# Performance work log

Measured on AMD Instinct MI355X. Metric: run time of the kernel, lower is better.

The kernel has to match this reference:

```python
import jax, jax.numpy as jnp
import numpy as np

B, H, S, D = 1, 8, 4096, 64


def setup_inputs() -> dict:
    key = jax.random.key(0)
    kq, kk, kv = jax.random.split(key, 3)
    Q = jax.random.normal(kq, (B, H, S, D), dtype=jnp.float32)
    K = jax.random.normal(kk, (B, H, S, D), dtype=jnp.float32)
    V = jax.random.normal(kv, (B, H, S, D), dtype=jnp.float32)
    # causal mask: 1 where attention allowed, 0 where blocked (matches masked_fill(mask==0, -inf))
    mask = jnp.tril(jnp.ones((S, S), dtype=jnp.int32))[None, None, :, :]
    return {"Q": Q, "K": K, "V": V, "mask": mask}


def reference(Q, K, V, mask):
    d_k = Q.shape[-1]
    scale = 1.0 / jnp.sqrt(jnp.asarray(d_k, Q.dtype))
    # [B,H,S,S] attention scores
    attn_score = jnp.einsum("bhqd,bhkd->bhqk", Q, K) * scale
    neg_inf = jnp.asarray(-jnp.inf, attn_score.dtype)
    attn_score = jnp.where(mask == 0, neg_inf, attn_score)
    attn_weight = jax.nn.softmax(attn_score, axis=-1)
    attn_output = jnp.einsum("bhqk,bhkd->bhqd", attn_weight, V)
    return attn_output
```

## Files before the change

### kernel.cpp

```cpp
#include <hip/hip_runtime.h>

#define S_LEN 4096
#define NHEAD 8
#define DDIM  64
#define NT    64
#define TILE_BYTES 8192
#define WS_NEEDED (2ull * NHEAD * NT * TILE_BYTES)

typedef __attribute__((ext_vector_type(4))) float f32x4;
typedef __attribute__((ext_vector_type(2))) float f32x2;
typedef __attribute__((ext_vector_type(8))) short bf16x8;

__device__ __forceinline__ unsigned cvt_pk(float lo, float hi) {
  unsigned r;
  asm("v_cvt_pk_bf16_f32 %0, %1, %2" : "=v"(r) : "v"(lo), "v"(hi));
  return r;
}
__device__ __forceinline__ float ex2(float x) {
  float r;
  asm("v_exp_f32 %0, %1" : "=v"(r) : "v"(x));
  return r;
}
__device__ __forceinline__ unsigned short f2bf(float f) {
  unsigned u = __float_as_uint(f);
  return (unsigned short)((u + 0x7fffu + ((u >> 16) & 1u)) >> 16);
}
__device__ __forceinline__ unsigned pk2(float a, float b) {
  return (unsigned)f2bf(a) | ((unsigned)f2bf(b) << 16);
}

__global__ __launch_bounds__(256)
void prepass(const float* __restrict__ K, const float* __restrict__ V,
             char* __restrict__ wsK, char* __restrict__ wsV) {
  const int bid = blockIdx.x;
  const int h = bid & 7, t = bid >> 3;
  const int tid = threadIdx.x;
  const size_t base = ((size_t)h * S_LEN + t * 64) * DDIM;
  char* ck = wsK + (size_t)(h * NT + t) * TILE_BYTES;
  char* cv = wsV + (size_t)(h * NT + t) * TILE_BYTES;
  {
    const int key = tid >> 2;
    const int fn = key >> 4, lq = key & 15;
#pragma unroll
    for (int p = 0; p < 2; ++p) {
      const int du = (tid & 3) + p * 4;
      const int kk = du >> 2, g = du & 3;
      const float* src = K + base + (size_t)key * DDIM + du * 8;
      f32x4 a = *(const f32x4*)src;
      f32x4 b = *(const f32x4*)(src + 4);
      uint4 u = {cvt_pk(a[0], a[1]), cvt_pk(a[2], a[3]),
                 cvt_pk(b[0], b[1]), cvt_pk(b[2], b[3])};
      *(uint4*)(ck + kk * 4096 + fn * 1024 + g * 256 + lq * 16) = u;
    }
  }
  {
    const int kgrp = tid >> 5;
    const int d0 = (tid & 31) * 2;
    const int kk = kgrp >> 2, g = kgrp & 3;
    float va[8], vb[8];
#pragma unroll
    for (int jj = 0; jj < 8; ++jj) {
      f32x2 x = *(const f32x2*)(V + base + (size_t)(kgrp * 8 + jj) * DDIM + d0);
      va[jj] = x[0]; vb[jj] = x[1];
    }
    uint4 ua = {cvt_pk(va[0], va[1]), cvt_pk(va[2], va[3]),
                cvt_pk(va[4], va[5]), cvt_pk(va[6], va[7])};
    uint4 ub = {cvt_pk(vb[0], vb[1]), cvt_pk(vb[2], vb[3]),
                cvt_pk(vb[4], vb[5]), cvt_pk(vb[6], vb[7])};
    const int fm0 = d0 >> 4, lq0 = d0 & 15;
    const int fm1 = (d0 + 1) >> 4, lq1 = (d0 + 1) & 15;
    *(uint4*)(cv + kk * 4096 + fm0 * 1024 + g * 256 + lq0 * 16) = ua;
    *(uint4*)(cv + kk * 4096 + fm1 * 1024 + g * 256 + lq1 * 16) = ub;
  }
}

__global__ __launch_bounds__(256)
void attn_fwd10(const float* __restrict__ Q, const char* __restrict__ wsK,
                const char* __restrict__ wsV, float* __restrict__ O) {
  __shared__ __align__(16) char pool[25344];

  const int tid = threadIdx.x, wave = tid >> 6, lane = tid & 63;
  const int g = lane >> 4, lq = lane & 15;
  const int bid = blockIdx.x, h = bid & 7, i = bid >> 3;
  const int qc = 127 - i;
  const int jd = qc >> 1;
  const int qbase = qc * 32;
  const int n = (jd >= wave) ? ((jd - wave) >> 2) + 1 : 0;

  const char* tK = wsK + (size_t)h * NT * TILE_BYTES;
  const char* tV = wsV + (size_t)h * NT * TILE_BYTES;
  const int foff = lane * 16;

  const float qsc = 0.125f * 1.44269504088896340736f;
  bf16x8 qf[2][2];
#pragma unroll
  for (int qh = 0; qh < 2; ++qh) {
    const float* qp = Q + ((size_t)h * S_LEN + qbase + qh * 16 + lq) * DDIM + g * 8;
#pragma unroll
    for (int kk = 0; kk < 2; ++kk) {
      f32x4 a = *(const f32x4*)(qp + kk * 32);
      f32x4 b = *(const f32x4*)(qp + kk * 32 + 4);
      uint4 u = {cvt_pk(a[0] * qsc, a[1] * qsc), cvt_pk(a[2] * qsc, a[3] * qsc),
                 cvt_pk(b[0] * qsc, b[1] * qsc), cvt_pk(b[2] * qsc, b[3] * qsc)};
      qf[qh][kk] = __builtin_bit_cast(bf16x8, u);
    }
  }

  f32x4 of0[4], of1[4];
#pragma unroll
  for (int fm = 0; fm < 4; ++fm) { of0[fm] = (f32x4){0,0,0,0}; of1[fm] = (f32x4){0,0,0,0}; }
  float l0 = 0.f, l1 = 0.f;

  char* pbase = pool + wave * 4608;
  const int prow = lq * 72;

  bf16x8 kf[4][2];
  if (n > 0) {
    const char* pk = tK + (size_t)wave * TILE_BYTES + foff;
#pragma unroll
    for (int fn = 0; fn < 4; ++fn)
#pragma unroll
      for (int kk = 0; kk < 2; ++kk)
        kf[fn][kk] = *(const bf16x8*)(pk + kk * 4096 + fn * 1024);
  }

  int j = wave;
  for (int it = 0; it < n; ++it, j += 4) {
    bf16x8 vf[4][2];
    const char* pv = tV + (size_t)j * TILE_BYTES + foff;
#pragma unroll
    for (int fm = 0; fm < 4; ++fm)
#pragma unroll
      for (int kk = 0; kk < 2; ++kk)
        vf[fm][kk] = *(const bf16x8*)(pv + kk * 4096 + fm * 1024);

    f32x4 s0[4], s1[4];
#pragma unroll
    for (int fn = 0; fn < 4; ++fn) {
      f32x4 a = (f32x4){0,0,0,0}, b = (f32x4){0,0,0,0};
      a = __builtin_amdgcn_mfma_f32_16x16x32_bf16(kf[fn][0], qf[0][0], a, 0, 0, 0);
      a = __builtin_amdgcn_mfma_f32_16x16x32_bf16(kf[fn][1], qf[0][1], a, 0, 0, 0);
      b = __builtin_amdgcn_mfma_f32_16x16x32_bf16(kf[fn][0], qf[1][0], b, 0, 0, 0);
      b = __builtin_amdgcn_mfma_f32_16x16x32_bf16(kf[fn][1], qf[1][1], b, 0, 0, 0);
      s0[fn] = a; s1[fn] = b;
    }

    if (it + 1 < n) {
      const char* pk = tK + (size_t)(j + 4) * TILE_BYTES + foff;
#pragma unroll
      for (int fn = 0; fn < 4; ++fn)
#pragma unroll
        for (int kk = 0; kk < 2; ++kk)
          kf[fn][kk] = *(const bf16x8*)(pk + kk * 4096 + fn * 1024);
    }

    if (j == jd) {
      const int koff = qbase - jd * 64;
#pragma unroll
      for (int fn = 0; fn < 4; ++fn)
#pragma unroll
        for (int rr = 0; rr < 4; ++rr) {
          const int key = fn * 16 + g * 4 + rr;
          if (key > koff + lq)      s0[fn][rr] = -__builtin_inff();
          if (key > koff + 16 + lq) s1[fn][rr] = -__builtin_inff();
        }
    }

    float rs0 = 0.f, rs1 = 0.f;
#pragma unroll
    for (int fn = 0; fn < 4; ++fn) {
      float a00 = ex2(s0[fn][0]), a01 = ex2(s0[fn][1]);
      float a02 = ex2(s0[fn][2]), a03 = ex2(s0[fn][3]);
      float a10 = ex2(s1[fn][0]), a11 = ex2(s1[fn][1]);
      float a12 = ex2(s1[fn][2]), a13 = ex2(s1[fn][3]);
      s0[fn][0] = a00; s0[fn][1] = a01; s0[fn][2] = a02; s0[fn][3] = a03;
      s1[fn][0] = a10; s1[fn][1] = a11; s1[fn][2] = a12; s1[fn][3] = a13;
      rs0 += (a00 + a01) + (a02 + a03);
      rs1 += (a10 + a11) + (a12 + a13);
    }
    l0 += rs0; l1 += rs1;

#pragma unroll
    for (int fn = 0; fn < 4; ++fn) {
      const int kk = fn >> 1;
      const int boff = ((fn & 1) * 2 + (g >> 1)) * 16 + (g & 1) * 8;
      unsigned long long w0 = (unsigned long long)cvt_pk(s0[fn][0], s0[fn][1])
                            | ((unsigned long long)cvt_pk(s0[fn][2], s0[fn][3]) << 32);
      unsigned long long w1 = (unsigned long long)cvt_pk(s1[fn][0], s1[fn][1])
                            | ((unsigned long long)cvt_pk(s1[fn][2], s1[fn][3]) << 32);
      *(unsigned long long*)(pbase + (kk * 2 + 0) * 1152 + prow + boff) = w0;
      *(unsigned long long*)(pbase + (kk * 2 + 1) * 1152 + prow + boff) = w1;
    }
    asm volatile("s_waitcnt lgkmcnt(0)" ::: "memory");

#pragma unroll
    for (int kk = 0; kk < 2; ++kk) {
      bf16x8 p0 = *(const bf16x8*)(pbase + (kk * 2 + 0) * 1152 + prow + g * 16);
      bf16x8 p1 = *(const bf16x8*)(pbase + (kk * 2 + 1) * 1152 + prow + g * 16);
#pragma unroll
      for (int fm = 0; fm < 4; ++fm) {
        of0[fm] = __builtin_amdgcn_mfma_f32_16x16x32_bf16(vf[fm][kk], p0, of0[fm], 0, 0, 0);
        of1[fm] = __builtin_amdgcn_mfma_f32_16x16x32_bf16(vf[fm][kk], p1, of1[fm], 0, 0, 0);
      }
    }
  }

  l0 += __shfl_xor(l0, 16); l0 += __shfl_xor(l0, 32);
  l1 += __shfl_xor(l1, 16); l1 += __shfl_xor(l1, 32);

  __syncthreads();
  if (wave < 3) {
    char* mb = pool + wave * 8192;
#pragma unroll
    for (int fm = 0; fm < 4; ++fm) {
      *(f32x4*)(mb + (fm * 2 + 0) * 1024 + g * 256 + lq * 16) = of0[fm];
      *(f32x4*)(mb + (fm * 2 + 1) * 1024 + g * 256 + lq * 16) = of1[fm];
    }
    if (g == 0) {
      f32x4 v = {l0, l1, 0.f, 0.f};
      *(f32x4*)(pool + 24576 + wave * 256 + lq * 16) = v;
    }
  }
  __syncthreads();
  if (wave == 3) {
    float den0 = l0, den1 = l1;
#pragma unroll
    for (int a = 0; a < 3; ++a) {
      f32x4 ml = *(const f32x4*)(pool + 24576 + a * 256 + lq * 16);
      den0 += ml[0];
      den1 += ml[1];
    }
    const float inv0 = 1.f / den0, inv1 = 1.f / den1;
    float* o0 = O + ((size_t)h * S_LEN + qbase + lq) * DDIM + g * 4;
    float* o1 = o0 + 16 * DDIM;
#pragma unroll
    for (int fm = 0; fm < 4; ++fm) {
      f32x4 r0 = of0[fm], r1 = of1[fm];
#pragma unroll
      for (int a = 0; a < 3; ++a) {
        r0 += *(const f32x4*)(pool + a * 8192 + (fm * 2 + 0) * 1024 + g * 256 + lq * 16);
        r1 += *(const f32x4*)(pool + a * 8192 + (fm * 2 + 1) * 1024 + g * 256 + lq * 16);
      }
      *(f32x4*)(o0 + fm * 16) = r0 * inv0;
      *(f32x4*)(o1 + fm * 16) = r1 * inv1;
    }
  }
}

__global__ __launch_bounds__(256, 2)
void attn_fwd_v1(const float* __restrict__ Q, const float* __restrict__ K,
                 const float* __restrict__ V, float* __restrict__ O) {
  __shared__ __align__(16) char kl[64 * 128];
  __shared__ __align__(16) char vt[64 * 128];
  __shared__ __align__(16) char pl[4 * 16 * 128];
  const int tid = threadIdx.x, wave = tid >> 6, lane = tid & 63;
  const int g = lane >> 4, lq = lane & 15;
  const int bid = blockIdx.x, h = bid & 7, i = bid >> 3;
  const int qt = (i & 1) ? (63 - (i >> 1)) : (i >> 1);
  const int qw = qt * 64 + wave * 16 + lq;
  const float* Qh = Q + ((size_t)h * S_LEN + qw) * DDIM;
  const float* Kh = K + (size_t)h * S_LEN * DDIM;
  const float* Vh = V + (size_t)h * S_LEN * DDIM;
  bf16x8 qf[2];
#pragma unroll
  for (int kk = 0; kk < 2; ++kk) {
    const float* p = Qh + g * 8 + kk * 32;
    f32x4 a = *(const f32x4*)p;
    f32x4 b = *(const f32x4*)(p + 4);
#pragma unroll
    for (int jj = 0; jj < 4; ++jj) {
      qf[kk][jj]     = (short)f2bf(a[jj] * 0.125f);
      qf[kk][jj + 4] = (short)f2bf(b[jj] * 0.125f);
    }
  }
  f32x4 of[4];
#pragma unroll
  for (int fm = 0; fm < 4; ++fm) of[fm] = (f32x4){0.f, 0.f, 0.f, 0.f};
  float mrun = -__builtin_inff(), lrun = 0.f;
  const int r16 = tid >> 4, c4 = tid & 15;
  const int vc = tid & 63, vkb = (tid >> 6) * 4;
  for (int j = 0; j <= qt; ++j) {
    const int k0 = j * 64;
    __syncthreads();
#pragma unroll
    for (int p = 0; p < 4; ++p) {
      const int rr = p * 16 + r16;
      f32x4 x = *(const f32x4*)(Kh + (size_t)(k0 + rr) * DDIM + c4 * 4);
      unsigned long long w = (unsigned long long)pk2(x[0], x[1])
                           | ((unsigned long long)pk2(x[2], x[3]) << 32);
      *(unsigned long long*)(kl + rr * 128 + ((c4 * 8) ^ ((rr & 7) << 4))) = w;
    }
#pragma unroll
    for (int p = 0; p < 4; ++p) {
      const int key = vkb + p * 16;
      const float* vp = Vh + (size_t)(k0 + key) * DDIM + vc;
      float v0 = vp[0], v1 = vp[DDIM], v2 = vp[2 * DDIM], v3 = vp[3 * DDIM];
      unsigned long long w = (unsigned long long)pk2(v0, v1)
                           | ((unsigned long long)pk2(v2, v3) << 32);
      *(unsigned long long*)(vt + vc * 128 + ((key * 2) ^ ((vc & 7) << 4))) = w;
    }
    __syncthreads();
    f32x4 sf[4];
#pragma unroll
    for (int fn = 0; fn < 4; ++fn) {
      f32x4 sv = (f32x4){0.f, 0.f, 0.f, 0.f};
#pragma unroll
      for (int kk = 0; kk < 2; ++kk) {
        const int krow = fn * 16 + lq;
        bf16x8 a = *(const bf16x8*)(kl + krow * 128 +
                                    ((g * 16 + kk * 64) ^ ((krow & 7) << 4)));
        sv = __builtin_amdgcn_mfma_f32_16x16x32_bf16(a, qf[kk], sv, 0, 0, 0);
      }
      sf[fn] = sv;
    }
    if (j == qt) {
      const int qrel = wave * 16 + lq;
#pragma unroll
      for (int fn = 0; fn < 4; ++fn)
#pragma unroll
        for (int rr = 0; rr < 4; ++rr)
          if (fn * 16 + g * 4 + rr > qrel) sf[fn][rr] = -__builtin_inff();
    }
    float mt = -__builtin_inff();
#pragma unroll
    for (int fn = 0; fn < 4; ++fn)
#pragma unroll
      for (int rr = 0; rr < 4; ++rr) mt = fmaxf(mt, sf[fn][rr]);
    mt = fmaxf(mt, __shfl_xor(mt, 16));
    mt = fmaxf(mt, __shfl_xor(mt, 32));
    const float mnew = fmaxf(mrun, mt);
    const float alpha = __expf(mrun - mnew);
    float rs = 0.f;
#pragma unroll
    for (int fn = 0; fn < 4; ++fn)
#pragma unroll
      for (int rr = 0; rr < 4; ++rr) {
        float p = __expf(sf[fn][rr] - mnew);
        sf[fn][rr] = p;
        rs += p;
      }
    rs += __shfl_xor(rs, 16);
    rs += __shfl_xor(rs, 32);
    mrun = mnew;
    lrun = lrun * alpha + rs;
#pragma unroll
    for (int fm = 0; fm < 4; ++fm) of[fm] *= alpha;
#pragma unroll
    for (int fn = 0; fn < 4; ++fn) {
      unsigned long long w = (unsigned long long)pk2(sf[fn][0], sf[fn][1])
                           | ((unsigned long long)pk2(sf[fn][2], sf[fn][3]) << 32);
      *(unsigned long long*)(pl + wave * 2048 + lq * 128 +
                             ((fn * 32 + g * 8) ^ ((lq & 7) << 4))) = w;
    }
    asm volatile("s_waitcnt lgkmcnt(0)" ::: "memory");
#pragma unroll
    for (int fm = 0; fm < 4; ++fm) {
#pragma unroll
      for (int kk = 0; kk < 2; ++kk) {
        const int vrow = fm * 16 + lq;
        bf16x8 av = *(const bf16x8*)(vt + vrow * 128 +
                                     ((g * 16 + kk * 64) ^ ((vrow & 7) << 4)));
        bf16x8 bp = *(const bf16x8*)(pl + wave * 2048 + lq * 128 +
                                     ((g * 16 + kk * 64) ^ ((lq & 7) << 4)));
        of[fm] = __builtin_amdgcn_mfma_f32_16x16x32_bf16(av, bp, of[fm], 0, 0, 0);
      }
    }
  }
  const float inv = 1.0f / lrun;
  float* orow = O + ((size_t)h * S_LEN + qw) * DDIM;
#pragma unroll
  for (int fm = 0; fm < 4; ++fm) {
    f32x4 o = of[fm] * inv;
    *(f32x4*)(orow + fm * 16 + g * 4) = o;
  }
}

extern "C" void kernel_launch(void* const* d_in, const int* in_sizes, int n_in,
                              void* d_out, int out_size, void* d_ws, size_t ws_size,
                              hipStream_t stream) {
  (void)in_sizes; (void)n_in; (void)out_size;
  const float* Q = (const float*)d_in[0];
  const float* K = (const float*)d_in[1];
  const float* V = (const float*)d_in[2];
  float* O = (float*)d_out;
  if (ws_size >= WS_NEEDED) {
    char* wsK = (char*)d_ws;
    char* wsV = wsK + (size_t)NHEAD * NT * TILE_BYTES;
    prepass<<<dim3(512), dim3(256), 0, stream>>>(K, V, wsK, wsV);
    attn_fwd10<<<dim3(1024), dim3(256), 0, stream>>>(Q, wsK, wsV, O);
  } else {
    attn_fwd_v1<<<dim3(512), dim3(256), 0, stream>>>(Q, K, V, O);
  }
}
```

Before: 44.30 us.

## Split causal attention KV range across two blocks and merge partials

Each 32-query chunk's key range is split into two halves processed by separate blocks (2048 blocks total). Each block writes unnormalized partial outputs and row sums to a workspace slot, and a new merge kernel sums the two partials and normalizes. The goal is to shorten the longest blocks on the causal tail and improve load balance and CU occupancy. The cost is an extra kernel launch plus a partial-result write and read through global memory. Because the kernel uses a fixed, shared exponent with no running max, partials can be summed directly without rescaling.

```diff
diff --git a/kernel.cpp b/kernel.cpp
--- a/kernel.cpp
+++ b/kernel.cpp
@@ -5,7 +5,10 @@
 #define DDIM  64
 #define NT    64
 #define TILE_BYTES 8192
-#define WS_NEEDED (2ull * NHEAD * NT * TILE_BYTES)
+#define SLOT_BYTES 8448
+#define NSEG 2048
+#define WS_KV (2ull * NHEAD * NT * TILE_BYTES)
+#define WS_SPLIT (WS_KV + (unsigned long long)NSEG * SLOT_BYTES)
 
 typedef __attribute__((ext_vector_type(4))) float f32x4;
 typedef __attribute__((ext_vector_type(2))) float f32x2;
@@ -20,13 +23,6 @@
   float r;
   asm("v_exp_f32 %0, %1" : "=v"(r) : "v"(x));
   return r;
-}
-__device__ __forceinline__ unsigned short f2bf(float f) {
-  unsigned u = __float_as_uint(f);
-  return (unsigned short)((u + 0x7fffu + ((u >> 16) & 1u)) >> 16);
-}
-__device__ __forceinline__ unsigned pk2(float a, float b) {
-  return (unsigned)f2bf(a) | ((unsigned)f2bf(b) << 16);
 }
 
 __global__ __launch_bounds__(256)
@@ -75,17 +71,23 @@
 }
 
 __global__ __launch_bounds__(256)
-void attn_fwd10(const float* __restrict__ Q, const char* __restrict__ wsK,
-                const char* __restrict__ wsV, float* __restrict__ O) {
+void attn_fwd11(const float* __restrict__ Q, const char* __restrict__ wsK,
+                const char* __restrict__ wsV, char* __restrict__ wsP) {
   __shared__ __align__(16) char pool[25344];
 
   const int tid = threadIdx.x, wave = tid >> 6, lane = tid & 63;
   const int g = lane >> 4, lq = lane & 15;
-  const int bid = blockIdx.x, h = bid & 7, i = bid >> 3;
-  const int qc = 127 - i;
+  const int bid = blockIdx.x;
+  const int h = bid & 7, idx = bid >> 3;
+  const int qc = 127 - (idx >> 1), half = idx & 1;
   const int jd = qc >> 1;
+  const int T = jd + 1;
+  const int Th = (T + 1) >> 1;
+  const int h0 = half ? Th : 0;
+  const int hend = half ? T : Th;
   const int qbase = qc * 32;
-  const int n = (jd >= wave) ? ((jd - wave) >> 2) + 1 : 0;
+  const int rem = hend - h0 - wave;
+  const int n = (rem > 0) ? ((rem + 3) >> 2) : 0;
 
   const char* tK = wsK + (size_t)h * NT * TILE_BYTES;
   const char* tV = wsV + (size_t)h * NT * TILE_BYTES;
@@ -116,7 +118,7 @@
 
   bf16x8 kf[4][2];
   if (n > 0) {
-    const char* pk = tK + (size_t)wave * TILE_BYTES + foff;
+    const char* pk = tK + (size_t)(h0 + wave) * TILE_BYTES + foff;
 #pragma unroll
     for (int fn = 0; fn < 4; ++fn)
 #pragma unroll
@@ -124,7 +126,7 @@
         kf[fn][kk] = *(const bf16x8*)(pk + kk * 4096 + fn * 1024);
   }
 
-  int j = wave;
+  int j = h0 + wave;
   for (int it = 0; it < n; ++it, j += 4) {
     bf16x8 vf[4][2];
     const char* pv = tV + (size_t)j * TILE_BYTES + foff;
@@ -230,6 +232,189 @@
       den0 += ml[0];
       den1 += ml[1];
     }
+    char* slot = wsP + (size_t)bid * SLOT_BYTES;
+#pragma unroll
+    for (int fm = 0; fm < 4; ++fm) {
+      f32x4 r0 = of0[fm], r1 = of1[fm];
+#pragma unroll
+      for (int a = 0; a < 3; ++a) {
+        r0 += *(const f32x4*)(pool + a * 8192 + (fm * 2 + 0) * 1024 + g * 256 + lq * 16);
+        r1 += *(const f32x4*)(pool + a * 8192 + (fm * 2 + 1) * 1024 + g * 256 + lq * 16);
+      }
+      const int d = (fm * 16 + g * 4) * 4;
+      *(f32x4*)(slot + lq * 256 + d) = r0;
+      *(f32x4*)(slot + (16 + lq) * 256 + d) = r1;
+    }
+    if (g == 0) {
+      *(float*)(slot + 8192 + lq * 4) = den0;
+      *(float*)(slot + 8192 + (16 + lq) * 4) = den1;
+    }
+  }
+}
+
+__global__ __launch_bounds__(256)
+void mergek(const char* __restrict__ wsP, float* __restrict__ O) {
+  const int mb = blockIdx.x;
+  const int h = mb & 7, c = mb >> 3;
+  const int qc = 127 - c;
+  const char* s0 = wsP + (size_t)(c * 16 + h) * SLOT_BYTES;
+  const char* s1 = s0 + 8 * SLOT_BYTES;
+  const int t = threadIdx.x;
+  const int q = t >> 3, d0 = (t & 7) * 8;
+  const float l = *(const float*)(s0 + 8192 + q * 4)
+                + *(const float*)(s1 + 8192 + q * 4);
+  const float inv = 1.f / l;
+  const int off = q * 256 + d0 * 4;
+  f32x4 a0 = *(const f32x4*)(s0 + off);
+  f32x4 a1 = *(const f32x4*)(s1 + off);
+  f32x4 b0 = *(const f32x4*)(s0 + off + 16);
+  f32x4 b1 = *(const f32x4*)(s1 + off + 16);
+  float* o = O + ((size_t)h * S_LEN + qc * 32 + q) * DDIM + d0;
+  *(f32x4*)o = (a0 + a1) * inv;
+  *(f32x4*)(o + 4) = (b0 + b1) * inv;
+}
+
+__global__ __launch_bounds__(256)
+void attn_fwd10(const float* __restrict__ Q, const char* __restrict__ wsK,
+                const char* __restrict__ wsV, float* __restrict__ O) {
+  __shared__ __align__(16) char pool[25344];
+  const int tid = threadIdx.x, wave = tid >> 6, lane = tid & 63;
+  const int g = lane >> 4, lq = lane & 15;
+  const int bid = blockIdx.x, h = bid & 7, i = bid >> 3;
+  const int qc = 127 - i;
+  const int jd = qc >> 1;
+  const int qbase = qc * 32;
+  const int n = (jd >= wave) ? ((jd - wave) >> 2) + 1 : 0;
+  const char* tK = wsK + (size_t)h * NT * TILE_BYTES;
+  const char* tV = wsV + (size_t)h * NT * TILE_BYTES;
+  const int foff = lane * 16;
+  const float qsc = 0.125f * 1.44269504088896340736f;
+  bf16x8 qf[2][2];
+#pragma unroll
+  for (int qh = 0; qh < 2; ++qh) {
+    const float* qp = Q + ((size_t)h * S_LEN + qbase + qh * 16 + lq) * DDIM + g * 8;
+#pragma unroll
+    for (int kk = 0; kk < 2; ++kk) {
+      f32x4 a = *(const f32x4*)(qp + kk * 32);
+      f32x4 b = *(const f32x4*)(qp + kk * 32 + 4);
+      uint4 u = {cvt_pk(a[0] * qsc, a[1] * qsc), cvt_pk(a[2] * qsc, a[3] * qsc),
+                 cvt_pk(b[0] * qsc, b[1] * qsc), cvt_pk(b[2] * qsc, b[3] * qsc)};
+      qf[qh][kk] = __builtin_bit_cast(bf16x8, u);
+    }
+  }
+  f32x4 of0[4], of1[4];
+#pragma unroll
+  for (int fm = 0; fm < 4; ++fm) { of0[fm] = (f32x4){0,0,0,0}; of1[fm] = (f32x4){0,0,0,0}; }
+  float l0 = 0.f, l1 = 0.f;
+  char* pbase = pool + wave * 4608;
+  const int prow = lq * 72;
+  bf16x8 kf[4][2];
+  if (n > 0) {
+    const char* pk = tK + (size_t)wave * TILE_BYTES + foff;
+#pragma unroll
+    for (int fn = 0; fn < 4; ++fn)
+#pragma unroll
+      for (int kk = 0; kk < 2; ++kk)
+        kf[fn][kk] = *(const bf16x8*)(pk + kk * 4096 + fn * 1024);
+  }
+  int j = wave;
+  for (int it = 0; it < n; ++it, j += 4) {
+    bf16x8 vf[4][2];
+    const char* pv = tV + (size_t)j * TILE_BYTES + foff;
+#pragma unroll
+    for (int fm = 0; fm < 4; ++fm)
+#pragma unroll
+      for (int kk = 0; kk < 2; ++kk)
+        vf[fm][kk] = *(const bf16x8*)(pv + kk * 4096 + fm * 1024);
+    f32x4 s0[4], s1[4];
+#pragma unroll
+    for (int fn = 0; fn < 4; ++fn) {
+      f32x4 a = (f32x4){0,0,0,0}, b = (f32x4){0,0,0,0};
+      a = __builtin_amdgcn_mfma_f32_16x16x32_bf16(kf[fn][0], qf[0][0], a, 0, 0, 0);
+      a = __builtin_amdgcn_mfma_f32_16x16x32_bf16(kf[fn][1], qf[0][1], a, 0, 0, 0);
+      b = __builtin_amdgcn_mfma_f32_16x16x32_bf16(kf[fn][0], qf[1][0], b, 0, 0, 0);
+      b = __builtin_amdgcn_mfma_f32_16x16x32_bf16(kf[fn][1], qf[1][1], b, 0, 0, 0);
+      s0[fn] = a; s1[fn] = b;
+    }
+    if (it + 1 < n) {
+      const char* pk = tK + (size_t)(j + 4) * TILE_BYTES + foff;
+#pragma unroll
+      for (int fn = 0; fn < 4; ++fn)
+#pragma unroll
+        for (int kk = 0; kk < 2; ++kk)
+          kf[fn][kk] = *(const bf16x8*)(pk + kk * 4096 + fn * 1024);
+    }
+    if (j == jd) {
+      const int koff = qbase - jd * 64;
+#pragma unroll
+      for (int fn = 0; fn < 4; ++fn)
+#pragma unroll
+        for (int rr = 0; rr < 4; ++rr) {
+          const int key = fn * 16 + g * 4 + rr;
+          if (key > koff + lq)      s0[fn][rr] = -__builtin_inff();
+          if (key > koff + 16 + lq) s1[fn][rr] = -__builtin_inff();
+        }
+    }
+    float rs0 = 0.f, rs1 = 0.f;
+#pragma unroll
+    for (int fn = 0; fn < 4; ++fn) {
+      float a00 = ex2(s0[fn][0]), a01 = ex2(s0[fn][1]);
+      float a02 = ex2(s0[fn][2]), a03 = ex2(s0[fn][3]);
+      float a10 = ex2(s1[fn][0]), a11 = ex2(s1[fn][1]);
+      float a12 = ex2(s1[fn][2]), a13 = ex2(s1[fn][3]);
+      s0[fn][0] = a00; s0[fn][1] = a01; s0[fn][2] = a02; s0[fn][3] = a03;
+      s1[fn][0] = a10; s1[fn][1] = a11; s1[fn][2] = a12; s1[fn][3] = a13;
+      rs0 += (a00 + a01) + (a02 + a03);
+      rs1 += (a10 + a11) + (a12 + a13);
+    }
+    l0 += rs0; l1 += rs1;
+#pragma unroll
+    for (int fn = 0; fn < 4; ++fn) {
+      const int kk = fn >> 1;
+      const int boff = ((fn & 1) * 2 + (g >> 1)) * 16 + (g & 1) * 8;
+      unsigned long long w0 = (unsigned long long)cvt_pk(s0[fn][0], s0[fn][1])
+                            | ((unsigned long long)cvt_pk(s0[fn][2], s0[fn][3]) << 32);
+      unsigned long long w1 = (unsigned long long)cvt_pk(s1[fn][0], s1[fn][1])
+                            | ((unsigned long long)cvt_pk(s1[fn][2], s1[fn][3]) << 32);
+      *(unsigned long long*)(pbase + (kk * 2 + 0) * 1152 + prow + boff) = w0;
+      *(unsigned long long*)(pbase + (kk * 2 + 1) * 1152 + prow + boff) = w1;
+    }
+    asm volatile("s_waitcnt lgkmcnt(0)" ::: "memory");
+#pragma unroll
+    for (int kk = 0; kk < 2; ++kk) {
+      bf16x8 p0 = *(const bf16x8*)(pbase + (kk * 2 + 0) * 1152 + prow + g * 16);
+      bf16x8 p1 = *(const bf16x8*)(pbase + (kk * 2 + 1) * 1152 + prow + g * 16);
+#pragma unroll
+      for (int fm = 0; fm < 4; ++fm) {
+        of0[fm] = __builtin_amdgcn_mfma_f32_16x16x32_bf16(vf[fm][kk], p0, of0[fm], 0, 0, 0);
+        of1[fm] = __builtin_amdgcn_mfma_f32_16x16x32_bf16(vf[fm][kk], p1, of1[fm], 0, 0, 0);
+      }
+    }
+  }
+  l0 += __shfl_xor(l0, 16); l0 += __shfl_xor(l0, 32);
+  l1 += __shfl_xor(l1, 16); l1 += __shfl_xor(l1, 32);
+  __syncthreads();
+  if (wave < 3) {
+    char* mb = pool + wave * 8192;
+#pragma unroll
+    for (int fm = 0; fm < 4; ++fm) {
+      *(f32x4*)(mb + (fm * 2 + 0) * 1024 + g * 256 + lq * 16) = of0[fm];
+      *(f32x4*)(mb + (fm * 2 + 1) * 1024 + g * 256 + lq * 16) = of1[fm];
+    }
+    if (g == 0) {
+      f32x4 v = {l0, l1, 0.f, 0.f};
+      *(f32x4*)(pool + 24576 + wave * 256 + lq * 16) = v;
+    }
+  }
+  __syncthreads();
+  if (wave == 3) {
+    float den0 = l0, den1 = l1;
+#pragma unroll
+    for (int a = 0; a < 3; ++a) {
+      f32x4 ml = *(const f32x4*)(pool + 24576 + a * 256 + lq * 16);
+      den0 += ml[0];
+      den1 += ml[1];
+    }
     const float inv0 = 1.f / den0, inv1 = 1.f / den1;
     float* o0 = O + ((size_t)h * S_LEN + qbase + lq) * DDIM + g * 4;
     float* o1 = o0 + 16 * DDIM;
@@ -244,134 +429,6 @@
       *(f32x4*)(o0 + fm * 16) = r0 * inv0;
       *(f32x4*)(o1 + fm * 16) = r1 * inv1;
     }
-  }
-}
-
-__global__ __launch_bounds__(256, 2)
-void attn_fwd_v1(const float* __restrict__ Q, const float* __restrict__ K,
-                 const float* __restrict__ V, float* __restrict__ O) {
-  __shared__ __align__(16) char kl[64 * 128];
-  __shared__ __align__(16) char vt[64 * 128];
-  __shared__ __align__(16) char pl[4 * 16 * 128];
-  const int tid = threadIdx.x, wave = tid >> 6, lane = tid & 63;
-  const int g = lane >> 4, lq = lane & 15;
-  const int bid = blockIdx.x, h = bid & 7, i = bid >> 3;
-  const int qt = (i & 1) ? (63 - (i >> 1)) : (i >> 1);
-  const int qw = qt * 64 + wave * 16 + lq;
-  const float* Qh = Q + ((size_t)h * S_LEN + qw) * DDIM;
-  const float* Kh = K + (size_t)h * S_LEN * DDIM;
-  const float* Vh = V + (size_t)h * S_LEN * DDIM;
-  bf16x8 qf[2];
-#pragma unroll
-  for (int kk = 0; kk < 2; ++kk) {
-    const float* p = Qh + g * 8 + kk * 32;
-    f32x4 a = *(const f32x4*)p;
-    f32x4 b = *(const f32x4*)(p + 4);
-#pragma unroll
-    for (int jj = 0; jj < 4; ++jj) {
-      qf[kk][jj]     = (short)f2bf(a[jj] * 0.125f);
-      qf[kk][jj + 4] = (short)f2bf(b[jj] * 0.125f);
-    }
-  }
-  f32x4 of[4];
-#pragma unroll
-  for (int fm = 0; fm < 4; ++fm) of[fm] = (f32x4){0.f, 0.f, 0.f, 0.f};
-  float mrun = -__builtin_inff(), lrun = 0.f;
-  const int r16 = tid >> 4, c4 = tid & 15;
-  const int vc = tid & 63, vkb = (tid >> 6) * 4;
-  for (int j = 0; j <= qt; ++j) {
-    const int k0 = j * 64;
-    __syncthreads();
-#pragma unroll
-    for (int p = 0; p < 4; ++p) {
-      const int rr = p * 16 + r16;
-      f32x4 x = *(const f32x4*)(Kh + (size_t)(k0 + rr) * DDIM + c4 * 4);
-      unsigned long long w = (unsigned long long)pk2(x[0], x[1])
-                           | ((unsigned long long)pk2(x[2], x[3]) << 32);
-      *(unsigned long long*)(kl + rr * 128 + ((c4 * 8) ^ ((rr & 7) << 4))) = w;
-    }
-#pragma unroll
-    for (int p = 0; p < 4; ++p) {
-      const int key = vkb + p * 16;
-      const float* vp = Vh + (size_t)(k0 + key) * DDIM + vc;
-      float v0 = vp[0], v1 = vp[DDIM], v2 = vp[2 * DDIM], v3 = vp[3 * DDIM];
-      unsigned long long w = (unsigned long long)pk2(v0, v1)
-                           | ((unsigned long long)pk2(v2, v3) << 32);
-      *(unsigned long long*)(vt + vc * 128 + ((key * 2) ^ ((vc & 7) << 4))) = w;
-    }
-    __syncthreads();
-    f32x4 sf[4];
-#pragma unroll
-    for (int fn = 0; fn < 4; ++fn) {
-      f32x4 sv = (f32x4){0.f, 0.f, 0.f, 0.f};
-#pragma unroll
-      for (int kk = 0; kk < 2; ++kk) {
-        const int krow = fn * 16 + lq;
-        bf16x8 a = *(const bf16x8*)(kl + krow * 128 +
-                                    ((g * 16 + kk * 64) ^ ((krow & 7) << 4)));
-        sv = __builtin_amdgcn_mfma_f32_16x16x32_bf16(a, qf[kk], sv, 0, 0, 0);
-      }
-      sf[fn] = sv;
-    }
-    if (j == qt) {
-      const int qrel = wave * 16 + lq;
-#pragma unroll
-      for (int fn = 0; fn < 4; ++fn)
-#pragma unroll
-        for (int rr = 0; rr < 4; ++rr)
-          if (fn * 16 + g * 4 + rr > qrel) sf[fn][rr] = -__builtin_inff();
-    }
-    float mt = -__builtin_inff();
-#pragma unroll
-    for (int fn = 0; fn < 4; ++fn)
-#pragma unroll
-      for (int rr = 0; rr < 4; ++rr) mt = fmaxf(mt, sf[fn][rr]);
-    mt = fmaxf(mt, __shfl_xor(mt, 16));
-    mt = fmaxf(mt, __shfl_xor(mt, 32));
-    const float mnew = fmaxf(mrun, mt);
-    const float alpha = __expf(mrun - mnew);
-    float rs = 0.f;
-#pragma unroll
-    for (int fn = 0; fn < 4; ++fn)
-#pragma unroll
-      for (int rr = 0; rr < 4; ++rr) {
-        float p = __expf(sf[fn][rr] - mnew);
-        sf[fn][rr] = p;
-        rs += p;
-      }
-    rs += __shfl_xor(rs, 16);
-    rs += __shfl_xor(rs, 32);
-    mrun = mnew;
-    lrun = lrun * alpha + rs;
-#pragma unroll
-    for (int fm = 0; fm < 4; ++fm) of[fm] *= alpha;
-#pragma unroll
-    for (int fn = 0; fn < 4; ++fn) {
-      unsigned long long w = (unsigned long long)pk2(sf[fn][0], sf[fn][1])
-                           | ((unsigned long long)pk2(sf[fn][2], sf[fn][3]) << 32);
-      *(unsigned long long*)(pl + wave * 2048 + lq * 128 +
-                             ((fn * 32 + g * 8) ^ ((lq & 7) << 4))) = w;
-    }
-    asm volatile("s_waitcnt lgkmcnt(0)" ::: "memory");
-#pragma unroll
-    for (int fm = 0; fm < 4; ++fm) {
-#pragma unroll
-      for (int kk = 0; kk < 2; ++kk) {
-        const int vrow = fm * 16 + lq;
-        bf16x8 av = *(const bf16x8*)(vt + vrow * 128 +
-                                     ((g * 16 + kk * 64) ^ ((vrow & 7) << 4)));
-        bf16x8 bp = *(const bf16x8*)(pl + wave * 2048 + lq * 128 +
-                                     ((g * 16 + kk * 64) ^ ((lq & 7) << 4)));
-        of[fm] = __builtin_amdgcn_mfma_f32_16x16x32_bf16(av, bp, of[fm], 0, 0, 0);
-      }
-    }
-  }
-  const float inv = 1.0f / lrun;
-  float* orow = O + ((size_t)h * S_LEN + qw) * DDIM;
-#pragma unroll
-  for (int fm = 0; fm < 4; ++fm) {
-    f32x4 o = of[fm] * inv;
-    *(f32x4*)(orow + fm * 16 + g * 4) = o;
   }
 }
 
@@ -383,12 +440,15 @@
   const float* K = (const float*)d_in[1];
   const float* V = (const float*)d_in[2];
   float* O = (float*)d_out;
-  if (ws_size >= WS_NEEDED) {
-    char* wsK = (char*)d_ws;
-    char* wsV = wsK + (size_t)NHEAD * NT * TILE_BYTES;
+  char* wsK = (char*)d_ws;
+  char* wsV = wsK + (size_t)NHEAD * NT * TILE_BYTES;
+  char* wsP = wsK + WS_KV;
+  if (ws_size >= WS_SPLIT) {
+    prepass<<<dim3(512), dim3(256), 0, stream>>>(K, V, wsK, wsV);
+    attn_fwd11<<<dim3(NSEG), dim3(256), 0, stream>>>(Q, wsK, wsV, wsP);
+    mergek<<<dim3(1024), dim3(256), 0, stream>>>(wsP, O);
+  } else {
     prepass<<<dim3(512), dim3(256), 0, stream>>>(K, V, wsK, wsV);
     attn_fwd10<<<dim3(1024), dim3(256), 0, stream>>>(Q, wsK, wsV, O);
-  } else {
-    attn_fwd_v1<<<dim3(512), dim3(256), 0, stream>>>(Q, K, V, O);
-  }
-}
+  }
+}
```

After: 53.34 us. +20.4%, slower.

## Software-pipeline QK^T of next tile with softmax and PV of current tile

Applied to the files above, without the earlier changes.

Restructures the per-wave loop so the S=QK^T MFMAs for the next key tile are issued before the PV MFMAs of the current tile. The K prefetch moves two tiles ahead and the V load moves one iteration ahead. This overlaps MFMA work with the exp/convert/LDS staging and hides global load latency. In exchange, more registers stay live (s0/s1 and the vf/kf prefetch buffers), which may lower occupancy or cause spills.

```diff
diff --git a/kernel.cpp b/kernel.cpp
--- a/kernel.cpp
+++ b/kernel.cpp
@@ -75,7 +75,7 @@
 }
 
 __global__ __launch_bounds__(256)
-void attn_fwd10(const float* __restrict__ Q, const char* __restrict__ wsK,
+void attn_fwd13(const float* __restrict__ Q, const char* __restrict__ wsK,
                 const char* __restrict__ wsV, float* __restrict__ O) {
   __shared__ __align__(16) char pool[25344];
 
@@ -114,27 +114,19 @@
   char* pbase = pool + wave * 4608;
   const int prow = lq * 72;
 
-  bf16x8 kf[4][2];
+  bf16x8 kf[4][2], vf[4][2];
+  f32x4 s0[4], s1[4];
+
   if (n > 0) {
     const char* pk = tK + (size_t)wave * TILE_BYTES + foff;
+    const char* pv = tV + (size_t)wave * TILE_BYTES + foff;
 #pragma unroll
     for (int fn = 0; fn < 4; ++fn)
 #pragma unroll
-      for (int kk = 0; kk < 2; ++kk)
+      for (int kk = 0; kk < 2; ++kk) {
         kf[fn][kk] = *(const bf16x8*)(pk + kk * 4096 + fn * 1024);
-  }
-
-  int j = wave;
-  for (int it = 0; it < n; ++it, j += 4) {
-    bf16x8 vf[4][2];
-    const char* pv = tV + (size_t)j * TILE_BYTES + foff;
-#pragma unroll
-    for (int fm = 0; fm < 4; ++fm)
-#pragma unroll
-      for (int kk = 0; kk < 2; ++kk)
-        vf[fm][kk] = *(const bf16x8*)(pv + kk * 4096 + fm * 1024);
-
-    f32x4 s0[4], s1[4];
+        vf[fn][kk] = *(const bf16x8*)(pv + kk * 4096 + fn * 1024);
+      }
 #pragma unroll
     for (int fn = 0; fn < 4; ++fn) {
       f32x4 a = (f32x4){0,0,0,0}, b = (f32x4){0,0,0,0};
@@ -144,15 +136,18 @@
       b = __builtin_amdgcn_mfma_f32_16x16x32_bf16(kf[fn][1], qf[1][1], b, 0, 0, 0);
       s0[fn] = a; s1[fn] = b;
     }
-
-    if (it + 1 < n) {
-      const char* pk = tK + (size_t)(j + 4) * TILE_BYTES + foff;
+    if (n > 1) {
+      const char* pk2 = tK + (size_t)(wave + 4) * TILE_BYTES + foff;
 #pragma unroll
       for (int fn = 0; fn < 4; ++fn)
 #pragma unroll
         for (int kk = 0; kk < 2; ++kk)
-          kf[fn][kk] = *(const bf16x8*)(pk + kk * 4096 + fn * 1024);
-    }
+          kf[fn][kk] = *(const bf16x8*)(pk2 + kk * 4096 + fn * 1024);
+    }
+  }
+
+  int j = wave;
+  for (int it = 0; it < n; ++it, j += 4) {
 
     if (j == jd) {
       const int koff = qbase - jd * 64;
@@ -173,24 +168,31 @@
       float a02 = ex2(s0[fn][2]), a03 = ex2(s0[fn][3]);
       float a10 = ex2(s1[fn][0]), a11 = ex2(s1[fn][1]);
       float a12 = ex2(s1[fn][2]), a13 = ex2(s1[fn][3]);
-      s0[fn][0] = a00; s0[fn][1] = a01; s0[fn][2] = a02; s0[fn][3] = a03;
-      s1[fn][0] = a10; s1[fn][1] = a11; s1[fn][2] = a12; s1[fn][3] = a13;
       rs0 += (a00 + a01) + (a02 + a03);
       rs1 += (a10 + a11) + (a12 + a13);
-    }
-    l0 += rs0; l1 += rs1;
-
-#pragma unroll
-    for (int fn = 0; fn < 4; ++fn) {
       const int kk = fn >> 1;
       const int boff = ((fn & 1) * 2 + (g >> 1)) * 16 + (g & 1) * 8;
-      unsigned long long w0 = (unsigned long long)cvt_pk(s0[fn][0], s0[fn][1])
-                            | ((unsigned long long)cvt_pk(s0[fn][2], s0[fn][3]) << 32);
-      unsigned long long w1 = (unsigned long long)cvt_pk(s1[fn][0], s1[fn][1])
-                            | ((unsigned long long)cvt_pk(s1[fn][2], s1[fn][3]) << 32);
+      unsigned long long w0 = (unsigned long long)cvt_pk(a00, a01)
+                            | ((unsigned long long)cvt_pk(a02, a03) << 32);
+      unsigned long long w1 = (unsigned long long)cvt_pk(a10, a11)
+                            | ((unsigned long long)cvt_pk(a12, a13) << 32);
       *(unsigned long long*)(pbase + (kk * 2 + 0) * 1152 + prow + boff) = w0;
       *(unsigned long long*)(pbase + (kk * 2 + 1) * 1152 + prow + boff) = w1;
     }
+    l0 += rs0; l1 += rs1;
+
+    if (it + 1 < n) {
+#pragma unroll
+      for (int fn = 0; fn < 4; ++fn) {
+        f32x4 a = (f32x4){0,0,0,0}, b = (f32x4){0,0,0,0};
+        a = __builtin_amdgcn_mfma_f32_16x16x32_bf16(kf[fn][0], qf[0][0], a, 0, 0, 0);
+        a = __builtin_amdgcn_mfma_f32_16x16x32_bf16(kf[fn][1], qf[0][1], a, 0, 0, 0);
+        b = __builtin_amdgcn_mfma_f32_16x16x32_bf16(kf[fn][0], qf[1][0], b, 0, 0, 0);
+        b = __builtin_amdgcn_mfma_f32_16x16x32_bf16(kf[fn][1], qf[1][1], b, 0, 0, 0);
+        s0[fn] = a; s1[fn] = b;
+      }
+    }
+
     asm volatile("s_waitcnt lgkmcnt(0)" ::: "memory");
 
 #pragma unroll
@@ -201,6 +203,23 @@
       for (int fm = 0; fm < 4; ++fm) {
         of0[fm] = __builtin_amdgcn_mfma_f32_16x16x32_bf16(vf[fm][kk], p0, of0[fm], 0, 0, 0);
         of1[fm] = __builtin_amdgcn_mfma_f32_16x16x32_bf16(vf[fm][kk], p1, of1[fm], 0, 0, 0);
+      }
+    }
+
+    if (it + 1 < n) {
+      const char* pv = tV + (size_t)(j + 4) * TILE_BYTES + foff;
+#pragma unroll
+      for (int fm = 0; fm < 4; ++fm)
+#pragma unroll
+        for (int kk = 0; kk < 2; ++kk)
+          vf[fm][kk] = *(const bf16x8*)(pv + kk * 4096 + fm * 1024);
+      if (it + 2 < n) {
+        const char* pk = tK + (size_t)(j + 8) * TILE_BYTES + foff;
+#pragma unroll
+        for (int fn = 0; fn < 4; ++fn)
+#pragma unroll
+          for (int kk = 0; kk < 2; ++kk)
+            kf[fn][kk] = *(const bf16x8*)(pk + kk * 4096 + fn * 1024);
       }
     }
   }
@@ -387,7 +406,7 @@
     char* wsK = (char*)d_ws;
     char* wsV = wsK + (size_t)NHEAD * NT * TILE_BYTES;
     prepass<<<dim3(512), dim3(256), 0, stream>>>(K, V, wsK, wsV);
-    attn_fwd10<<<dim3(1024), dim3(256), 0, stream>>>(Q, wsK, wsV, O);
+    attn_fwd13<<<dim3(1024), dim3(256), 0, stream>>>(Q, wsK, wsV, O);
   } else {
     attn_fwd_v1<<<dim3(512), dim3(256), 0, stream>>>(Q, K, V, O);
   }
```

After: 43.30 us. 1.02x faster.

## Pair causal query chunks per block, software-pipeline QK, compute row sums via MFMA

Applied to the files above, without the earlier changes.

Each block now processes two query chunks (p and 127-p) so causal work is balanced across 512 blocks instead of 1024 unevenly sized ones. The inner loop is software-pipelined: the next tile's QK^T MFMAs are issued between the exp/LDS store and the PV MFMAs, with K/V loads prefetched one to two iterations ahead. Row sums are accumulated by an MFMA against a ones vector, which replaces the scalar adds and shuffles. The cost is more registers, an extra barrier per chunk, and serialization of the two chunks within a block.

```diff
diff --git a/kernel.cpp b/kernel.cpp
--- a/kernel.cpp
+++ b/kernel.cpp
@@ -75,175 +75,184 @@
 }
 
 __global__ __launch_bounds__(256)
-void attn_fwd10(const float* __restrict__ Q, const char* __restrict__ wsK,
+void attn_fwd16(const float* __restrict__ Q, const char* __restrict__ wsK,
                 const char* __restrict__ wsV, float* __restrict__ O) {
   __shared__ __align__(16) char pool[25344];
 
   const int tid = threadIdx.x, wave = tid >> 6, lane = tid & 63;
   const int g = lane >> 4, lq = lane & 15;
-  const int bid = blockIdx.x, h = bid & 7, i = bid >> 3;
-  const int qc = 127 - i;
-  const int jd = qc >> 1;
-  const int qbase = qc * 32;
-  const int n = (jd >= wave) ? ((jd - wave) >> 2) + 1 : 0;
+  const int bid = blockIdx.x, h = bid & 7, p = bid >> 3;
 
   const char* tK = wsK + (size_t)h * NT * TILE_BYTES;
   const char* tV = wsV + (size_t)h * NT * TILE_BYTES;
   const int foff = lane * 16;
-
   const float qsc = 0.125f * 1.44269504088896340736f;
-  bf16x8 qf[2][2];
-#pragma unroll
-  for (int qh = 0; qh < 2; ++qh) {
-    const float* qp = Q + ((size_t)h * S_LEN + qbase + qh * 16 + lq) * DDIM + g * 8;
-#pragma unroll
-    for (int kk = 0; kk < 2; ++kk) {
-      f32x4 a = *(const f32x4*)(qp + kk * 32);
-      f32x4 b = *(const f32x4*)(qp + kk * 32 + 4);
-      uint4 u = {cvt_pk(a[0] * qsc, a[1] * qsc), cvt_pk(a[2] * qsc, a[3] * qsc),
-                 cvt_pk(b[0] * qsc, b[1] * qsc), cvt_pk(b[2] * qsc, b[3] * qsc)};
-      qf[qh][kk] = __builtin_bit_cast(bf16x8, u);
-    }
-  }
-
-  f32x4 of0[4], of1[4];
-#pragma unroll
-  for (int fm = 0; fm < 4; ++fm) { of0[fm] = (f32x4){0,0,0,0}; of1[fm] = (f32x4){0,0,0,0}; }
-  float l0 = 0.f, l1 = 0.f;
-
   char* pbase = pool + wave * 4608;
   const int prow = lq * 72;
 
-  bf16x8 kf[4][2];
-  if (n > 0) {
-    const char* pk = tK + (size_t)wave * TILE_BYTES + foff;
-#pragma unroll
-    for (int fn = 0; fn < 4; ++fn)
-#pragma unroll
-      for (int kk = 0; kk < 2; ++kk)
-        kf[fn][kk] = *(const bf16x8*)(pk + kk * 4096 + fn * 1024);
-  }
-
-  int j = wave;
-  for (int it = 0; it < n; ++it, j += 4) {
-    bf16x8 vf[4][2];
-    const char* pv = tV + (size_t)j * TILE_BYTES + foff;
-#pragma unroll
-    for (int fm = 0; fm < 4; ++fm)
-#pragma unroll
-      for (int kk = 0; kk < 2; ++kk)
-        vf[fm][kk] = *(const bf16x8*)(pv + kk * 4096 + fm * 1024);
-
+  bf16x8 ones;
+#pragma unroll
+  for (int z = 0; z < 8; ++z) ones[z] = (short)0x3F80;
+
+  for (int cc = 0; cc < 2; ++cc) {
+    const int qc = cc ? (127 - p) : p;
+    const int jd = qc >> 1;
+    const int qbase = qc * 32;
+    const int n = (jd >= wave) ? ((jd - wave) >> 2) + 1 : 0;
+
+    bf16x8 qf[2][2];
+#pragma unroll
+    for (int qh = 0; qh < 2; ++qh) {
+      const float* qp = Q + ((size_t)h * S_LEN + qbase + qh * 16 + lq) * DDIM + g * 8;
+#pragma unroll
+      for (int kk = 0; kk < 2; ++kk) {
+        f32x4 a = *(const f32x4*)(qp + kk * 32);
+        f32x4 b = *(const f32x4*)(qp + kk * 32 + 4);
+        uint4 u = {cvt_pk(a[0] * qsc, a[1] * qsc), cvt_pk(a[2] * qsc, a[3] * qsc),
+                   cvt_pk(b[0] * qsc, b[1] * qsc), cvt_pk(b[2] * qsc, b[3] * qsc)};
+        qf[qh][kk] = __builtin_bit_cast(bf16x8, u);
+      }
+    }
+
+    f32x4 of0[4], of1[4];
+#pragma unroll
+    for (int fm = 0; fm < 4; ++fm) { of0[fm] = (f32x4){0,0,0,0}; of1[fm] = (f32x4){0,0,0,0}; }
+    f32x4 lac0 = (f32x4){0,0,0,0}, lac1 = (f32x4){0,0,0,0};
+
+    bf16x8 kf[4][2], vf[4][2];
     f32x4 s0[4], s1[4];
-#pragma unroll
-    for (int fn = 0; fn < 4; ++fn) {
-      f32x4 a = (f32x4){0,0,0,0}, b = (f32x4){0,0,0,0};
-      a = __builtin_amdgcn_mfma_f32_16x16x32_bf16(kf[fn][0], qf[0][0], a, 0, 0, 0);
-      a = __builtin_amdgcn_mfma_f32_16x16x32_bf16(kf[fn][1], qf[0][1], a, 0, 0, 0);
-      b = __builtin_amdgcn_mfma_f32_16x16x32_bf16(kf[fn][0], qf[1][0], b, 0, 0, 0);
-      b = __builtin_amdgcn_mfma_f32_16x16x32_bf16(kf[fn][1], qf[1][1], b, 0, 0, 0);
-      s0[fn] = a; s1[fn] = b;
-    }
-
-    if (it + 1 < n) {
-      const char* pk = tK + (size_t)(j + 4) * TILE_BYTES + foff;
+
+    const char* kptr = tK + (size_t)wave * TILE_BYTES + foff;
+    const char* vptr = tV + (size_t)wave * TILE_BYTES + foff;
+
+    auto LOADK = [&]() {
 #pragma unroll
       for (int fn = 0; fn < 4; ++fn)
 #pragma unroll
         for (int kk = 0; kk < 2; ++kk)
-          kf[fn][kk] = *(const bf16x8*)(pk + kk * 4096 + fn * 1024);
-    }
-
-    if (j == jd) {
-      const int koff = qbase - jd * 64;
-#pragma unroll
-      for (int fn = 0; fn < 4; ++fn)
-#pragma unroll
-        for (int rr = 0; rr < 4; ++rr) {
-          const int key = fn * 16 + g * 4 + rr;
-          if (key > koff + lq)      s0[fn][rr] = -__builtin_inff();
-          if (key > koff + 16 + lq) s1[fn][rr] = -__builtin_inff();
+          kf[fn][kk] = *(const bf16x8*)(kptr + kk * 4096 + fn * 1024);
+      kptr += 4 * TILE_BYTES;
+    };
+    auto LOADV = [&]() {
+#pragma unroll
+      for (int fm = 0; fm < 4; ++fm)
+#pragma unroll
+        for (int kk = 0; kk < 2; ++kk)
+          vf[fm][kk] = *(const bf16x8*)(vptr + kk * 4096 + fm * 1024);
+      vptr += 4 * TILE_BYTES;
+    };
+    auto QK = [&]() {
+#pragma unroll
+      for (int fn = 0; fn < 4; ++fn) {
+        f32x4 a = (f32x4){0,0,0,0}, b = (f32x4){0,0,0,0};
+        a = __builtin_amdgcn_mfma_f32_16x16x32_bf16(kf[fn][0], qf[0][0], a, 0, 0, 0);
+        a = __builtin_amdgcn_mfma_f32_16x16x32_bf16(kf[fn][1], qf[0][1], a, 0, 0, 0);
+        b = __builtin_amdgcn_mfma_f32_16x16x32_bf16(kf[fn][0], qf[1][0], b, 0, 0, 0);
+        b = __builtin_amdgcn_mfma_f32_16x16x32_bf16(kf[fn][1], qf[1][1], b, 0, 0, 0);
+        s0[fn] = a; s1[fn] = b;
+      }
+    };
+
+    if (n > 0) {
+      LOADK();
+      LOADV();
+      QK();
+      if (n > 1) LOADK();
+    }
+
+    int j = wave;
+    for (int it = 0; it < n; ++it, j += 4) {
+      if (j == jd) {
+        const int koff = qbase - jd * 64;
+#pragma unroll
+        for (int fn = 0; fn < 4; ++fn)
+#pragma unroll
+          for (int rr = 0; rr < 4; ++rr) {
+            const int key = fn * 16 + g * 4 + rr;
+            if (key > koff + lq)      s0[fn][rr] = -__builtin_inff();
+            if (key > koff + 16 + lq) s1[fn][rr] = -__builtin_inff();
+          }
+      }
+
+#pragma unroll
+      for (int fn = 0; fn < 4; ++fn) {
+        float a00 = ex2(s0[fn][0]), a01 = ex2(s0[fn][1]);
+        float a02 = ex2(s0[fn][2]), a03 = ex2(s0[fn][3]);
+        float a10 = ex2(s1[fn][0]), a11 = ex2(s1[fn][1]);
+        float a12 = ex2(s1[fn][2]), a13 = ex2(s1[fn][3]);
+        const int kk = fn >> 1;
+        const int boff = ((fn & 1) * 2 + (g >> 1)) * 16 + (g & 1) * 8;
+        unsigned long long w0 = (unsigned long long)cvt_pk(a00, a01)
+                              | ((unsigned long long)cvt_pk(a02, a03) << 32);
+        unsigned long long w1 = (unsigned long long)cvt_pk(a10, a11)
+                              | ((unsigned long long)cvt_pk(a12, a13) << 32);
+        *(unsigned long long*)(pbase + (kk * 2 + 0) * 1152 + prow + boff) = w0;
+        *(unsigned long long*)(pbase + (kk * 2 + 1) * 1152 + prow + boff) = w1;
+      }
+
+      if (it + 1 < n) QK();
+
+      asm volatile("s_waitcnt lgkmcnt(0)" ::: "memory");
+
+#pragma unroll
+      for (int kk = 0; kk < 2; ++kk) {
+        bf16x8 p0 = *(const bf16x8*)(pbase + (kk * 2 + 0) * 1152 + prow + g * 16);
+        bf16x8 p1 = *(const bf16x8*)(pbase + (kk * 2 + 1) * 1152 + prow + g * 16);
+        lac0 = __builtin_amdgcn_mfma_f32_16x16x32_bf16(ones, p0, lac0, 0, 0, 0);
+        lac1 = __builtin_amdgcn_mfma_f32_16x16x32_bf16(ones, p1, lac1, 0, 0, 0);
+#pragma unroll
+        for (int fm = 0; fm < 4; ++fm) {
+          of0[fm] = __builtin_amdgcn_mfma_f32_16x16x32_bf16(vf[fm][kk], p0, of0[fm], 0, 0, 0);
+          of1[fm] = __builtin_amdgcn_mfma_f32_16x16x32_bf16(vf[fm][kk], p1, of1[fm], 0, 0, 0);
         }
-    }
-
-    float rs0 = 0.f, rs1 = 0.f;
-#pragma unroll
-    for (int fn = 0; fn < 4; ++fn) {
-      float a00 = ex2(s0[fn][0]), a01 = ex2(s0[fn][1]);
-      float a02 = ex2(s0[fn][2]), a03 = ex2(s0[fn][3]);
-      float a10 = ex2(s1[fn][0]), a11 = ex2(s1[fn][1]);
-      float a12 = ex2(s1[fn][2]), a13 = ex2(s1[fn][3]);
-      s0[fn][0] = a00; s0[fn][1] = a01; s0[fn][2] = a02; s0[fn][3] = a03;
-      s1[fn][0] = a10; s1[fn][1] = a11; s1[fn][2] = a12; s1[fn][3] = a13;
-      rs0 += (a00 + a01) + (a02 + a03);
-      rs1 += (a10 + a11) + (a12 + a13);
-    }
-    l0 += rs0; l1 += rs1;
-
-#pragma unroll
-    for (int fn = 0; fn < 4; ++fn) {
-      const int kk = fn >> 1;
-      const int boff = ((fn & 1) * 2 + (g >> 1)) * 16 + (g & 1) * 8;
-      unsigned long long w0 = (unsigned long long)cvt_pk(s0[fn][0], s0[fn][1])
-                            | ((unsigned long long)cvt_pk(s0[fn][2], s0[fn][3]) << 32);
-      unsigned long long w1 = (unsigned long long)cvt_pk(s1[fn][0], s1[fn][1])
-                            | ((unsigned long long)cvt_pk(s1[fn][2], s1[fn][3]) << 32);
-      *(unsigned long long*)(pbase + (kk * 2 + 0) * 1152 + prow + boff) = w0;
-      *(unsigned long long*)(pbase + (kk * 2 + 1) * 1152 + prow + boff) = w1;
-    }
-    asm volatile("s_waitcnt lgkmcnt(0)" ::: "memory");
-
-#pragma unroll
-    for (int kk = 0; kk < 2; ++kk) {
-      bf16x8 p0 = *(const bf16x8*)(pbase + (kk * 2 + 0) * 1152 + prow + g * 16);
-      bf16x8 p1 = *(const bf16x8*)(pbase + (kk * 2 + 1) * 1152 + prow + g * 16);
+      }
+
+      if (it + 1 < n) {
+        LOADV();
+        if (it + 2 < n) LOADK();
+      }
+    }
+
+    const float l0 = lac0[0], l1 = lac1[0];
+
+    __syncthreads();
+    if (wave < 3) {
+      char* mb = pool + wave * 8192;
 #pragma unroll
       for (int fm = 0; fm < 4; ++fm) {
-        of0[fm] = __builtin_amdgcn_mfma_f32_16x16x32_bf16(vf[fm][kk], p0, of0[fm], 0, 0, 0);
-        of1[fm] = __builtin_amdgcn_mfma_f32_16x16x32_bf16(vf[fm][kk], p1, of1[fm], 0, 0, 0);
-      }
-    }
-  }
-
-  l0 += __shfl_xor(l0, 16); l0 += __shfl_xor(l0, 32);
-  l1 += __shfl_xor(l1, 16); l1 += __shfl_xor(l1, 32);
-
-  __syncthreads();
-  if (wave < 3) {
-    char* mb = pool + wave * 8192;
-#pragma unroll
-    for (int fm = 0; fm < 4; ++fm) {
-      *(f32x4*)(mb + (fm * 2 + 0) * 1024 + g * 256 + lq * 16) = of0[fm];
-      *(f32x4*)(mb + (fm * 2 + 1) * 1024 + g * 256 + lq * 16) = of1[fm];
-    }
-    if (g == 0) {
-      f32x4 v = {l0, l1, 0.f, 0.f};
-      *(f32x4*)(pool + 24576 + wave * 256 + lq * 16) = v;
-    }
-  }
-  __syncthreads();
-  if (wave == 3) {
-    float den0 = l0, den1 = l1;
-#pragma unroll
-    for (int a = 0; a < 3; ++a) {
-      f32x4 ml = *(const f32x4*)(pool + 24576 + a * 256 + lq * 16);
-      den0 += ml[0];
-      den1 += ml[1];
-    }
-    const float inv0 = 1.f / den0, inv1 = 1.f / den1;
-    float* o0 = O + ((size_t)h * S_LEN + qbase + lq) * DDIM + g * 4;
-    float* o1 = o0 + 16 * DDIM;
-#pragma unroll
-    for (int fm = 0; fm < 4; ++fm) {
-      f32x4 r0 = of0[fm], r1 = of1[fm];
+        *(f32x4*)(mb + (fm * 2 + 0) * 1024 + g * 256 + lq * 16) = of0[fm];
+        *(f32x4*)(mb + (fm * 2 + 1) * 1024 + g * 256 + lq * 16) = of1[fm];
+      }
+      if (g == 0) {
+        f32x4 v = {l0, l1, 0.f, 0.f};
+        *(f32x4*)(pool + 24576 + wave * 256 + lq * 16) = v;
+      }
+    }
+    __syncthreads();
+    if (wave == 3) {
+      float den0 = l0, den1 = l1;
 #pragma unroll
       for (int a = 0; a < 3; ++a) {
-        r0 += *(const f32x4*)(pool + a * 8192 + (fm * 2 + 0) * 1024 + g * 256 + lq * 16);
-        r1 += *(const f32x4*)(pool + a * 8192 + (fm * 2 + 1) * 1024 + g * 256 + lq * 16);
-      }
-      *(f32x4*)(o0 + fm * 16) = r0 * inv0;
-      *(f32x4*)(o1 + fm * 16) = r1 * inv1;
-    }
+        f32x4 ml = *(const f32x4*)(pool + 24576 + a * 256 + lq * 16);
+        den0 += ml[0];
+        den1 += ml[1];
+      }
+      const float inv0 = 1.f / den0, inv1 = 1.f / den1;
+      float* o0 = O + ((size_t)h * S_LEN + qbase + lq) * DDIM + g * 4;
+      float* o1 = o0 + 16 * DDIM;
+#pragma unroll
+      for (int fm = 0; fm < 4; ++fm) {
+        f32x4 r0 = of0[fm], r1 = of1[fm];
+#pragma unroll
+        for (int a = 0; a < 3; ++a) {
+          r0 += *(const f32x4*)(pool + a * 8192 + (fm * 2 + 0) * 1024 + g * 256 + lq * 16);
+          r1 += *(const f32x4*)(pool + a * 8192 + (fm * 2 + 1) * 1024 + g * 256 + lq * 16);
+        }
+        *(f32x4*)(o0 + fm * 16) = r0 * inv0;
+        *(f32x4*)(o1 + fm * 16) = r1 * inv1;
+      }
+    }
+    __syncthreads();
   }
 }
 
@@ -387,7 +396,7 @@
     char* wsK = (char*)d_ws;
     char* wsV = wsK + (size_t)NHEAD * NT * TILE_BYTES;
     prepass<<<dim3(512), dim3(256), 0, stream>>>(K, V, wsK, wsV);
-    attn_fwd10<<<dim3(1024), dim3(256), 0, stream>>>(Q, wsK, wsV, O);
+    attn_fwd16<<<dim3(512), dim3(256), 0, stream>>>(Q, wsK, wsV, O);
   } else {
     attn_fwd_v1<<<dim3(512), dim3(256), 0, stream>>>(Q, K, V, O);
   }
```

New measurement: 51.99 us. 17.3% more time.
